# Kernel optimization log

Hardware: AMD Instinct MI355X
Metric: run time of the kernel (lower is better)

The kernel has to match this reference:

```python
import jax, jax.numpy as jnp
import numpy as np

IN_F = 1024
OUT_F = 1024
B, S = 8, 4096


def _pack_ternary(tern):
    # encoding: -1 -> 0, 0 -> 1, +1 -> 2; 4 values per byte, matching torch pack_ternary_weights
    enc = (tern + 1.0).astype(jnp.int32).reshape(-1)  # length divisible by 4 here
    return (enc[0::4] | (enc[1::4] << 2) | (enc[2::4] << 4) | (enc[3::4] << 6)).astype(jnp.int32)


def setup_inputs() -> dict:
    key = jax.random.key(0)
    kx, kw = jax.random.split(key)
    x = jax.random.normal(kx, (B, S, IN_F), dtype=jnp.float32)
    w = jax.random.normal(kw, (OUT_F, IN_F), dtype=jnp.float32) * 0.02
    # quantize_weights_158bit
    scale = jnp.maximum(jnp.mean(jnp.abs(w)), 1e-5)
    wn = w / scale
    tern = jnp.sign(wn) * (jnp.abs(wn) > 0.5).astype(jnp.float32)
    packed = _pack_ternary(tern)
    bias = jnp.zeros((OUT_F,), dtype=jnp.float32)
    return {"x": x, "packed_weight": packed, "weight_scale": scale.reshape(1), "bias": bias}


def reference(x, packed_weight, weight_scale, bias):
    n = OUT_F * IN_F
    shifts = jnp.array([0, 2, 4, 6], dtype=jnp.int32)
    # Faithful to original unpack_ternary_weights: concatenate bit-planes, then truncate.
    # (This is a permutation of the packed order, replicated deliberately.)
    enc = ((packed_weight[None, :] >> shifts[:, None]) & 3).reshape(-1)[:n]
    w = (enc.astype(jnp.float32) - 1.0).reshape(OUT_F, IN_F) * weight_scale  # dequant ternary
    # training path: INT8 per-token activation fake-quant
    act_scale = 127.0 / jnp.maximum(jnp.max(jnp.abs(x), axis=-1, keepdims=True), 1e-5)
    x_dq = jnp.clip(jnp.round(x * act_scale), -128.0, 127.0) / act_scale
    return jnp.einsum('bsi,oi->bso', x_dq, w) + bias
```

## Files before the change

### kernel.cpp

```cpp
#include <hip/hip_runtime.h>
#include <hip/hip_bf16.h>
#include <stdint.h>

typedef int i32x4 __attribute__((ext_vector_type(4)));

constexpr int IN_F = 1024;
constexpr int OUT_F = 1024;
constexpr int M_TOT = 8 * 4096;
constexpr int K_TOT = IN_F;
constexpr int N_TOT = OUT_F;

__global__ __launch_bounds__(256) void quant_kernel(
    const float* __restrict__ x,
    const float* __restrict__ wscale,
    int8_t* __restrict__ q,
    float* __restrict__ inv_row)
{
    const int row = blockIdx.x;
    const int t = threadIdx.x;
    const float4 v = reinterpret_cast<const float4*>(x + (size_t)row * IN_F)[t];
    float m = fmaxf(fmaxf(fabsf(v.x), fabsf(v.y)), fmaxf(fabsf(v.z), fabsf(v.w)));
    #pragma unroll
    for (int off = 32; off > 0; off >>= 1)
        m = fmaxf(m, __shfl_xor(m, off));
    __shared__ float smax[4];
    if ((t & 63) == 0) smax[t >> 6] = m;
    __syncthreads();
    m = fmaxf(fmaxf(smax[0], smax[1]), fmaxf(smax[2], smax[3]));
    const float a = fmaxf(m, 1e-5f);
    const float as = 127.0f / a;

    char4 o;
    o.x = (char)(int)fminf(fmaxf(rintf(v.x * as), -128.0f), 127.0f);
    o.y = (char)(int)fminf(fmaxf(rintf(v.y * as), -128.0f), 127.0f);
    o.z = (char)(int)fminf(fmaxf(rintf(v.z * as), -128.0f), 127.0f);
    o.w = (char)(int)fminf(fmaxf(rintf(v.w * as), -128.0f), 127.0f);
    reinterpret_cast<char4*>(q + (size_t)row * IN_F)[t] = o;
    if (t == 0) inv_row[row] = (a / 127.0f) * wscale[0];
}

__global__ __launch_bounds__(256) void unpack_kernel(
    const int* __restrict__ packed,
    int8_t* __restrict__ wt2)
{
    const int o = blockIdx.x;
    const int t = threadIdx.x;
    const int k0 = t * 4;
    const int sh = (o >> 8) * 2;
    const int pbase = ((o & 255) << 10) + k0;
    const int4 pw = *reinterpret_cast<const int4*>(packed + pbase);
    char4 r;
    r.x = (char)(((pw.x >> sh) & 3) - 1);
    r.y = (char)(((pw.y >> sh) & 3) - 1);
    r.z = (char)(((pw.z >> sh) & 3) - 1);
    r.w = (char)(((pw.w >> sh) & 3) - 1);
    const int addr = (k0 >> 6) * 65536 + o * 64 + ((k0 >> 4) & 3) * 16 + (k0 & 15);
    *reinterpret_cast<char4*>(wt2 + addr) = r;
}

constexpr int BM = 256, BN = 128, BK = 64;
constexpr int NT = K_TOT / BK;

__global__ __launch_bounds__(512, 4) void gemm_kernel(
    const int8_t* __restrict__ qa,
    const int8_t* __restrict__ wb2,
    const float* __restrict__ inv_row,
    const float* __restrict__ bias,
    float* __restrict__ out)
{
    int bid = blockIdx.x;
    bid = (bid & 7) * ((int)gridDim.x >> 3) + (bid >> 3);
    const int tm = bid >> 3;
    const int tn = bid & 7;

    const int tid = threadIdx.x;
    const int lane = tid & 63;
    const int wid = tid >> 6;
    const int wr = wid >> 1;
    const int wc = wid & 1;

    __shared__ int8_t ldsA[3 * 256 * 64];

    const int rowA0 = tm * BM;
    const int rowB0 = tn * BN;
    const int frow = lane & 15;
    const int fq = lane >> 4;

    i32x4 acc[4][4] = {};

    const int r0 = tid >> 2;
    const int scc0 = (tid & 3) ^ ((r0 >> 1) & 3);
    const int8_t* srcA0 = qa + (size_t)(rowA0 + r0) * K_TOT + scc0 * 16;
    const int dA0 = tid * 16, dA1 = (512 + tid) * 16;

    auto stageA = [&](int slot, int kt) {
        __builtin_amdgcn_global_load_lds(
            (const __attribute__((address_space(1))) void*)(srcA0 + kt * BK),
            (__attribute__((address_space(3))) void*)&ldsA[slot * 16384 + dA0], 16, 0, 0);
        __builtin_amdgcn_global_load_lds(
            (const __attribute__((address_space(1))) void*)(srcA0 + (size_t)128 * K_TOT + kt * BK),
            (__attribute__((address_space(3))) void*)&ldsA[slot * 16384 + dA1], 16, 0, 0);
    };

    auto ldA = [&](int slot, int mf) -> i32x4 {
        const int r = wr * 64 + mf * 16 + frow;
        const int ch = fq ^ ((r >> 1) & 3);
        return *reinterpret_cast<const i32x4*>(&ldsA[slot * 16384 + r * 64 + ch * 16]);
    };

    const int8_t* wbBase = wb2 + (size_t)(rowB0 + wc * 64 + frow) * 64 + fq * 16;
    auto loadB = [&](int kt, i32x4 (&b)[4]) {
        #pragma unroll
        for (int nf = 0; nf < 4; ++nf)
            b[nf] = *reinterpret_cast<const i32x4*>(wbBase + kt * 65536 + nf * 1024);
    };

    i32x4 bX[4], bY[4];

    stageA(0, 0);
    stageA(1, 1);
    loadB(0, bX);
    loadB(1, bY);

    auto body = [&](int T, i32x4 (&bCur)[4]) {
        const int s = T % 3;
        if (T < NT - 1) asm volatile("s_waitcnt vmcnt(10)" ::: "memory");
        else            asm volatile("s_waitcnt vmcnt(4)" ::: "memory");
        __builtin_amdgcn_s_barrier();

        i32x4 aF[4];
        #pragma unroll
        for (int mf = 0; mf < 4; ++mf) aF[mf] = ldA(s, mf);

        if (T + 2 < NT) stageA((T + 2) % 3, T + 2);

        asm volatile("s_waitcnt lgkmcnt(0)" ::: "memory");
        __builtin_amdgcn_sched_barrier(0);
        __builtin_amdgcn_s_setprio(1);
        #pragma unroll
        for (int mf = 0; mf < 4; ++mf)
            #pragma unroll
            for (int nf = 0; nf < 4; ++nf)
                acc[mf][nf] = __builtin_amdgcn_mfma_i32_16x16x64_i8(
                    aF[mf], bCur[nf], acc[mf][nf], 0, 0, 0);
        __builtin_amdgcn_s_setprio(0);

        if (T + 2 < NT) loadB(T + 2, bCur);
    };

    for (int t2 = 0; t2 < NT; t2 += 2) {
        body(t2, bX);
        body(t2 + 1, bY);
    }

    #pragma unroll
    for (int mf = 0; mf < 4; ++mf) {
        #pragma unroll
        for (int j = 0; j < 4; ++j) {
            const int gm = rowA0 + wr * 64 + mf * 16 + fq * 4 + j;
            const float sc = inv_row[gm];
            #pragma unroll
            for (int nf = 0; nf < 4; ++nf) {
                const int gn = rowB0 + wc * 64 + nf * 16 + frow;
                out[(size_t)gm * N_TOT + gn] = (float)acc[mf][nf][j] * sc + bias[gn];
            }
        }
    }
}

extern "C" void kernel_launch(void* const* d_in, const int* in_sizes, int n_in,
                              void* d_out, int out_size, void* d_ws, size_t ws_size,
                              hipStream_t stream) {
    const float* x = (const float*)d_in[0];
    const int* packed = (const int*)d_in[1];
    const float* wscale = (const float*)d_in[2];
    const float* bias = (const float*)d_in[3];
    float* out = (float*)d_out;

    int8_t* q = (int8_t*)d_ws;
    int8_t* wt2 = (int8_t*)((char*)d_ws + (size_t)M_TOT * K_TOT);
    float* inv_row = (float*)((char*)d_ws + (size_t)M_TOT * K_TOT + (size_t)N_TOT * K_TOT);

    quant_kernel<<<M_TOT, 256, 0, stream>>>(x, wscale, q, inv_row);
    unpack_kernel<<<OUT_F, 256, 0, stream>>>(packed, wt2);
    gemm_kernel<<<(M_TOT / BM) * (N_TOT / BN), 512, 0, stream>>>(q, wt2, inv_row, bias, out);
}
```

Before: 98.51 us.

## Reshape GEMM tile to 128x256 with BK=128 and single-buffered B fragments

The int8 GEMM tile changes from 256x128 with BK=64 to 128x256 with BK=128. Warps are rearranged to 2x4 and the A LDS staging now uses an 8-chunk XOR swizzle over 128-byte rows. Each iteration runs two k-substeps of MFMAs, which halves the loop trip count and barrier count. In exchange, B fragments drop from two register sets prefetched two tiles ahead to one set loaded right after compute, so global load latency for B is less hidden.

```diff
diff --git a/kernel.cpp b/kernel.cpp
--- a/kernel.cpp
+++ b/kernel.cpp
@@ -58,7 +58,7 @@
     *reinterpret_cast<char4*>(wt2 + addr) = r;
 }
 
-constexpr int BM = 256, BN = 128, BK = 64;
+constexpr int BM = 128, BN = 256, BK = 128;
 constexpr int NT = K_TOT / BK;
 
 __global__ __launch_bounds__(512, 4) void gemm_kernel(
@@ -70,16 +70,16 @@
 {
     int bid = blockIdx.x;
     bid = (bid & 7) * ((int)gridDim.x >> 3) + (bid >> 3);
-    const int tm = bid >> 3;
-    const int tn = bid & 7;
+    const int tm = bid >> 2;
+    const int tn = bid & 3;
 
     const int tid = threadIdx.x;
     const int lane = tid & 63;
     const int wid = tid >> 6;
-    const int wr = wid >> 1;
-    const int wc = wid & 1;
+    const int wr = wid >> 2;
+    const int wc = wid & 3;
 
-    __shared__ int8_t ldsA[3 * 256 * 64];
+    __shared__ int8_t ldsA[3][128 * 128];
 
     const int rowA0 = tm * BM;
     const int rowB0 = tn * BN;
@@ -88,52 +88,53 @@
 
     i32x4 acc[4][4] = {};
 
-    const int r0 = tid >> 2;
-    const int scc0 = (tid & 3) ^ ((r0 >> 1) & 3);
-    const int8_t* srcA0 = qa + (size_t)(rowA0 + r0) * K_TOT + scc0 * 16;
+    const int rl0 = tid >> 3;
+    const int scc0 = (tid & 7) ^ (rl0 & 7);
+    const int8_t* srcA0 = qa + (size_t)(rowA0 + rl0) * K_TOT + scc0 * 16;
     const int dA0 = tid * 16, dA1 = (512 + tid) * 16;
 
     auto stageA = [&](int slot, int kt) {
         __builtin_amdgcn_global_load_lds(
             (const __attribute__((address_space(1))) void*)(srcA0 + kt * BK),
-            (__attribute__((address_space(3))) void*)&ldsA[slot * 16384 + dA0], 16, 0, 0);
+            (__attribute__((address_space(3))) void*)&ldsA[slot][dA0], 16, 0, 0);
         __builtin_amdgcn_global_load_lds(
-            (const __attribute__((address_space(1))) void*)(srcA0 + (size_t)128 * K_TOT + kt * BK),
-            (__attribute__((address_space(3))) void*)&ldsA[slot * 16384 + dA1], 16, 0, 0);
+            (const __attribute__((address_space(1))) void*)(srcA0 + (size_t)64 * K_TOT + kt * BK),
+            (__attribute__((address_space(3))) void*)&ldsA[slot][dA1], 16, 0, 0);
     };
 
-    auto ldA = [&](int slot, int mf) -> i32x4 {
-        const int r = wr * 64 + mf * 16 + frow;
-        const int ch = fq ^ ((r >> 1) & 3);
-        return *reinterpret_cast<const i32x4*>(&ldsA[slot * 16384 + r * 64 + ch * 16]);
+    auto ldA = [&](int slot, int mf, int ks) -> i32x4 {
+        const int local = wr * 64 + mf * 16 + frow;
+        const int ch = (ks * 4 + fq) ^ (local & 7);
+        return *reinterpret_cast<const i32x4*>(&ldsA[slot][local * 128 + ch * 16]);
     };
 
     const int8_t* wbBase = wb2 + (size_t)(rowB0 + wc * 64 + frow) * 64 + fq * 16;
-    auto loadB = [&](int kt, i32x4 (&b)[4]) {
+    i32x4 bF[4][2];
+    auto loadB = [&](int T) {
         #pragma unroll
         for (int nf = 0; nf < 4; ++nf)
-            b[nf] = *reinterpret_cast<const i32x4*>(wbBase + kt * 65536 + nf * 1024);
+            #pragma unroll
+            for (int ks = 0; ks < 2; ++ks)
+                bF[nf][ks] = *reinterpret_cast<const i32x4*>(
+                    wbBase + (size_t)(T * 2 + ks) * 65536 + nf * 1024);
     };
-
-    i32x4 bX[4], bY[4];
 
     stageA(0, 0);
     stageA(1, 1);
-    loadB(0, bX);
-    loadB(1, bY);
+    loadB(0);
 
-    auto body = [&](int T, i32x4 (&bCur)[4]) {
-        const int s = T % 3;
+    #pragma unroll 1
+    for (int T = 0; T < NT; ++T) {
+        const int sa = T % 3;
         if (T < NT - 1) asm volatile("s_waitcnt vmcnt(10)" ::: "memory");
-        else            asm volatile("s_waitcnt vmcnt(4)" ::: "memory");
+        else            asm volatile("s_waitcnt vmcnt(0)" ::: "memory");
         __builtin_amdgcn_s_barrier();
 
         i32x4 aF[4];
+
         #pragma unroll
-        for (int mf = 0; mf < 4; ++mf) aF[mf] = ldA(s, mf);
-
+        for (int mf = 0; mf < 4; ++mf) aF[mf] = ldA(sa, mf, 0);
         if (T + 2 < NT) stageA((T + 2) % 3, T + 2);
-
         asm volatile("s_waitcnt lgkmcnt(0)" ::: "memory");
         __builtin_amdgcn_sched_barrier(0);
         __builtin_amdgcn_s_setprio(1);
@@ -142,15 +143,23 @@
             #pragma unroll
             for (int nf = 0; nf < 4; ++nf)
                 acc[mf][nf] = __builtin_amdgcn_mfma_i32_16x16x64_i8(
-                    aF[mf], bCur[nf], acc[mf][nf], 0, 0, 0);
+                    aF[mf], bF[nf][0], acc[mf][nf], 0, 0, 0);
         __builtin_amdgcn_s_setprio(0);
 
-        if (T + 2 < NT) loadB(T + 2, bCur);
-    };
+        #pragma unroll
+        for (int mf = 0; mf < 4; ++mf) aF[mf] = ldA(sa, mf, 1);
+        asm volatile("s_waitcnt lgkmcnt(0)" ::: "memory");
+        __builtin_amdgcn_sched_barrier(0);
+        __builtin_amdgcn_s_setprio(1);
+        #pragma unroll
+        for (int mf = 0; mf < 4; ++mf)
+            #pragma unroll
+            for (int nf = 0; nf < 4; ++nf)
+                acc[mf][nf] = __builtin_amdgcn_mfma_i32_16x16x64_i8(
+                    aF[mf], bF[nf][1], acc[mf][nf], 0, 0, 0);
+        __builtin_amdgcn_s_setprio(0);
 
-    for (int t2 = 0; t2 < NT; t2 += 2) {
-        body(t2, bX);
-        body(t2 + 1, bY);
+        if (T + 1 < NT) loadB(T + 1);
     }
 
     #pragma unroll
```

Result: faster. 94.15 us (-4.4%).
